# Kernel tuning notes

Hardware: AMD Instinct MI355X
Metric: run time of the kernel (lower is better)

The kernel has to match this reference:

```python
import jax, jax.numpy as jnp
import numpy as np

B, S, IN_DIM, OUT_DIM, HID = 16, 256, 128, 128, 512


def setup_inputs() -> dict:
    key = jax.random.key(0)
    ks = jax.random.split(key, 7)
    x = jax.random.normal(ks[0], (B, S, IN_DIM), dtype=jnp.float32)
    # hypernet linear 1: input_dim -> hyper_hidden_dim
    W1 = jax.random.normal(ks[1], (IN_DIM, HID), dtype=jnp.float32) / np.sqrt(IN_DIM)
    b1 = jax.random.normal(ks[2], (HID,), dtype=jnp.float32) * 0.01
    # hypernet linear 2: hyper_hidden_dim -> input_dim * output_dim
    W2 = jax.random.normal(ks[3], (HID, IN_DIM * OUT_DIM), dtype=jnp.float32) / np.sqrt(HID)
    b2 = jax.random.normal(ks[4], (IN_DIM * OUT_DIM,), dtype=jnp.float32) * 0.01
    # final fc: output_dim -> output_dim
    Wfc = jax.random.normal(ks[5], (OUT_DIM, OUT_DIM), dtype=jnp.float32) / np.sqrt(OUT_DIM)
    bfc = jax.random.normal(ks[6], (OUT_DIM,), dtype=jnp.float32) * 0.01
    return {"x": x, "W1": W1, "b1": b1, "W2": W2, "b2": b2, "Wfc": Wfc, "bfc": bfc}


def reference(x, W1, b1, W2, b2, Wfc, bfc):
    # hypernet: per-token generated weight matrix Wx [B,S,IN,OUT]
    h = jax.nn.relu(jnp.einsum('bsi,ih->bsh', x, W1) + b1)
    Wx = (jnp.einsum('bsh,ho->bso', h, W2) + b2).reshape(x.shape[0], x.shape[1], IN_DIM, OUT_DIM)
    # batched vector-matrix product per (b,s), then sum over s -> [B, OUT]
    y = jnp.einsum('bsi,bsio->bo', x, Wx)
    return y @ Wfc + bfc
```

## Files before the change

### kernel.cpp

```cpp
#include <hip/hip_runtime.h>


typedef __attribute__((ext_vector_type(8))) short     s16x8;
typedef __attribute__((ext_vector_type(8))) unsigned short u16x8;
typedef __attribute__((ext_vector_type(4))) float     f32x4;

__device__ __forceinline__ unsigned short f2bf(float f) {
    union { float f; unsigned int u; } v; v.f = f;
    unsigned int r = v.u + 0x7FFFu + ((v.u >> 16) & 1u);
    return (unsigned short)(r >> 16);
}
__device__ __forceinline__ float bf2f(unsigned short u) {
    union { unsigned int u; float f; } v; v.u = ((unsigned int)u) << 16;
    return v.f;
}

#define OFF_MP   0
#define OFF_PART 2097152
#define OFF_SXP  3145728

__global__ __launch_bounds__(256) void k_AB(const float* __restrict__ x,
        const float* __restrict__ W1, const float* __restrict__ b1,
        float* __restrict__ Mp, float* __restrict__ sxp) {
    __shared__ unsigned short xA[128][136];
    __shared__ unsigned short Ws[128][136];
    __shared__ unsigned short xTl[128][136];
    __shared__ float Wt[128][33];
    __shared__ float b1s[128];
    const int tid = threadIdx.x;
    const int b = blockIdx.x >> 3, sh = (blockIdx.x >> 2) & 1, hb = blockIdx.x & 3;

    {
        const int r = tid >> 1, q = tid & 1;
        const float* xrow = &x[(size_t)(b * 256 + sh * 128 + r) * 128 + q * 64];
        #pragma unroll
        for (int m = 0; m < 8; ++m) {
            const float4 v0 = *(const float4*)&xrow[m * 8];
            const float4 v1 = *(const float4*)&xrow[m * 8 + 4];
            unsigned short t8[8] __attribute__((aligned(16))) = {
                f2bf(v0.x), f2bf(v0.y), f2bf(v0.z), f2bf(v0.w),
                f2bf(v1.x), f2bf(v1.y), f2bf(v1.z), f2bf(v1.w)};
            *(u16x8*)&xA[r][q * 64 + m * 8] = *(u16x8*)t8;
        }
        if (tid < 128) b1s[tid] = b1[hb * 128 + tid];
    }
    for (int hq = 0; hq < 4; ++hq) {
        __syncthreads();
        #pragma unroll
        for (int p = 0; p < 16; ++p) {
            const int flat = p * 256 + tid;
            const int i = flat >> 5, hc = flat & 31;
            Wt[i][hc] = W1[(size_t)i * 512 + hb * 128 + hq * 32 + hc];
        }
        __syncthreads();
        {
            const int h2 = tid >> 3, pt = tid & 7;
            unsigned short t16[16] __attribute__((aligned(16)));
            #pragma unroll
            for (int m = 0; m < 16; ++m)
                t16[m] = f2bf(Wt[pt * 16 + m][h2]);
            *(u16x8*)&Ws[hq * 32 + h2][pt * 16]     = *(u16x8*)&t16[0];
            *(u16x8*)&Ws[hq * 32 + h2][pt * 16 + 8] = *(u16x8*)&t16[8];
        }
    }
    __syncthreads();

    const int w = tid >> 6, lane = tid & 63;
    const int wr = w >> 1, wc = w & 1;
    const int l15 = lane & 15, kl = lane >> 4;
    f32x4 zero = {0.f, 0.f, 0.f, 0.f};

    f32x4 acc[4][4];
    #pragma unroll
    for (int i = 0; i < 4; ++i)
        #pragma unroll
        for (int j = 0; j < 4; ++j) acc[i][j] = zero;
    #pragma unroll
    for (int ks = 0; ks < 4; ++ks) {
        s16x8 a[4], bb[4];
        #pragma unroll
        for (int f = 0; f < 4; ++f) {
            a[f]  = *(const s16x8*)&xA[wr * 64 + f * 16 + l15][ks * 32 + kl * 8];
            bb[f] = *(const s16x8*)&Ws[wc * 64 + f * 16 + l15][ks * 32 + kl * 8];
        }
        #pragma unroll
        for (int fr = 0; fr < 4; ++fr)
            #pragma unroll
            for (int fc = 0; fc < 4; ++fc)
                acc[fr][fc] = __builtin_amdgcn_mfma_f32_16x16x32_bf16(a[fr], bb[fc], acc[fr][fc], 0, 0, 0);
    }
    __syncthreads();

    {
        const int i = tid >> 1, q = tid & 1;
        float sacc = 0.f;
        unsigned short t64[64] __attribute__((aligned(16)));
        #pragma unroll
        for (int m = 0; m < 64; ++m) {
            const unsigned short u = xA[q * 64 + m][i];
            sacc += bf2f(u);
            t64[m] = u;
        }
        #pragma unroll
        for (int v = 0; v < 8; ++v)
            *(u16x8*)&xTl[i][q * 64 + v * 8] = *(u16x8*)&t64[v * 8];
        if (hb == 0)
            sxp[(size_t)((sh * 2 + q) * 16 + b) * 128 + i] = sacc;
    }
    __syncthreads();

    unsigned short (*hts)[136] = xA;
    #pragma unroll
    for (int fr = 0; fr < 4; ++fr)
        #pragma unroll
        for (int fc = 0; fc < 4; ++fc)
            #pragma unroll
            for (int j = 0; j < 4; ++j) {
                const int tok = wr * 64 + fr * 16 + kl * 4 + j;
                const int hid = wc * 64 + fc * 16 + l15;
                const float v = acc[fr][fc][j] + b1s[hid];
                hts[hid][tok] = f2bf(v > 0.f ? v : 0.f);
            }
    __syncthreads();

    f32x4 acc2[4][4];
    #pragma unroll
    for (int i = 0; i < 4; ++i)
        #pragma unroll
        for (int j = 0; j < 4; ++j) acc2[i][j] = zero;
    #pragma unroll
    for (int ks = 0; ks < 4; ++ks) {
        s16x8 a[4], bb[4];
        #pragma unroll
        for (int f = 0; f < 4; ++f) {
            a[f]  = *(const s16x8*)&hts[wr * 64 + f * 16 + l15][ks * 32 + kl * 8];
            bb[f] = *(const s16x8*)&xTl[wc * 64 + f * 16 + l15][ks * 32 + kl * 8];
        }
        #pragma unroll
        for (int fr = 0; fr < 4; ++fr)
            #pragma unroll
            for (int fc = 0; fc < 4; ++fc)
                acc2[fr][fc] = __builtin_amdgcn_mfma_f32_16x16x32_bf16(a[fr], bb[fc], acc2[fr][fc], 0, 0, 0);
    }
    const size_t mpbase = (size_t)sh * (16 * 65536) + (size_t)b * 65536;
    #pragma unroll
    for (int fr = 0; fr < 4; ++fr)
        #pragma unroll
        for (int fc = 0; fc < 4; ++fc)
            #pragma unroll
            for (int j = 0; j < 4; ++j) {
                const int h = hb * 128 + wr * 64 + fr * 16 + kl * 4 + j;
                const int i = wc * 64 + fc * 16 + l15;
                Mp[mpbase + (size_t)h * 128 + i] = acc2[fr][fc][j];
            }
}

__global__ __launch_bounds__(256) void k_C(const float* __restrict__ Mp,
        const float* __restrict__ W2, float* __restrict__ part) {
    __shared__ float Ms[16][128];
    const int tid = threadIdx.x;
    const int p = blockIdx.x;
    const int k0 = p * 128;
    #pragma unroll
    for (int r = 0; r < 8; ++r) {
        const int flat = r * 256 + tid;
        const int b = flat >> 7, kk = flat & 127;
        Ms[b][kk] = Mp[(size_t)b * 65536 + k0 + kk]
                  + Mp[(size_t)(16 + b) * 65536 + k0 + kk];
    }
    __syncthreads();
    const int o2 = (tid & 63) * 2;
    const int g  = tid >> 6;
    float acc[4][2] = {};
    #pragma unroll 8
    for (int kk = 0; kk < 128; ++kk) {
        const float2 w = *(const float2*)&W2[(size_t)(k0 + kk) * 128 + o2];
        #pragma unroll
        for (int bb = 0; bb < 4; ++bb) {
            const float m = Ms[g * 4 + bb][kk];
            acc[bb][0] += m * w.x;
            acc[bb][1] += m * w.y;
        }
    }
    #pragma unroll
    for (int bb = 0; bb < 4; ++bb) {
        float2 v = {acc[bb][0], acc[bb][1]};
        *(float2*)&part[(size_t)(p * 16 + g * 4 + bb) * 128 + o2] = v;
    }
}

__global__ __launch_bounds__(1024) void k_D(const float* __restrict__ part,
        const float* __restrict__ sxp, const float* __restrict__ b2,
        const float* __restrict__ Wfc, const float* __restrict__ bfc,
        float* __restrict__ out) {
    __shared__ float sh[8][128];
    __shared__ float sxs[128];
    __shared__ float ysum[128];
    __shared__ float ysh[128];
    const int b = blockIdx.x;
    const int t = threadIdx.x & 127;
    const int g = threadIdx.x >> 7;
    float y = 0.f;
    #pragma unroll 8
    for (int pp = g * 64; pp < g * 64 + 64; ++pp)
        y += part[(size_t)(pp * 16 + b) * 128 + t];
    sh[g][t] = y;
    __syncthreads();
    if (g == 0) {
        float yy = sh[0][t];
        #pragma unroll
        for (int j = 1; j < 8; ++j) yy += sh[j][t];
        ysum[t] = yy;
        sxs[t] = sxp[(size_t)(0 * 16 + b) * 128 + t] + sxp[(size_t)(1 * 16 + b) * 128 + t]
               + sxp[(size_t)(2 * 16 + b) * 128 + t] + sxp[(size_t)(3 * 16 + b) * 128 + t];
    }
    __syncthreads();
    float yb = 0.f;
    #pragma unroll
    for (int i = g * 16; i < g * 16 + 16; ++i)
        yb += sxs[i] * b2[i * 128 + t];
    sh[g][t] = yb;
    __syncthreads();
    if (g == 0) {
        float yy = ysum[t];
        #pragma unroll
        for (int j = 0; j < 8; ++j) yy += sh[j][t];
        ysh[t] = yy;
    }
    __syncthreads();
    float f = 0.f;
    #pragma unroll
    for (int oo = g * 16; oo < g * 16 + 16; ++oo)
        f += ysh[oo] * Wfc[oo * 128 + t];
    sh[g][t] = f;
    __syncthreads();
    if (g == 0) {
        float s = bfc[t];
        #pragma unroll
        for (int j = 0; j < 8; ++j) s += sh[j][t];
        out[b * 128 + t] = s;
    }
}

extern "C" void kernel_launch(void* const* d_in, const int* in_sizes, int n_in,
                              void* d_out, int out_size, void* d_ws, size_t ws_size,
                              hipStream_t stream) {
    const float* x   = (const float*)d_in[0];
    const float* W1  = (const float*)d_in[1];
    const float* b1  = (const float*)d_in[2];
    const float* W2  = (const float*)d_in[3];
    const float* b2  = (const float*)d_in[4];
    const float* Wfc = (const float*)d_in[5];
    const float* bfc = (const float*)d_in[6];
    float* ws  = (float*)d_ws;
    float* Mp   = ws + OFF_MP;
    float* part = ws + OFF_PART;
    float* sxp  = ws + OFF_SXP;
    float* out  = (float*)d_out;

    k_AB<<<128, 256, 0, stream>>>(x, W1, b1, Mp, sxp);
    k_C <<<512, 256, 0, stream>>>(Mp, W2, part);
    k_D <<<16, 1024, 0, stream>>>(part, sxp, b2, Wfc, bfc, out);
}
```

Before: 34.75 us.

## Split hidden dim finer in k_AB, alias shared memory, vectorize k_C W2 loads

k_AB now gives each block 64 hidden units instead of 128, doubling the grid to 256 blocks so the GPU's many CUs are better filled. Shared buffers are packed into one aliased byte array (Wt overlaps xTl, hts overlaps Ws) to shrink LDS per block. k_C switches to float4 W2 loads with 2 batches per thread instead of float2 with 4. The trade-off is that the x tile load, transpose and bf16 conversion are now repeated in twice as many blocks.

```diff
diff --git a/kernel.cpp b/kernel.cpp
--- a/kernel.cpp
+++ b/kernel.cpp
@@ -22,13 +22,18 @@
 __global__ __launch_bounds__(256) void k_AB(const float* __restrict__ x,
         const float* __restrict__ W1, const float* __restrict__ b1,
         float* __restrict__ Mp, float* __restrict__ sxp) {
-    __shared__ unsigned short xA[128][136];
-    __shared__ unsigned short Ws[128][136];
-    __shared__ unsigned short xTl[128][136];
-    __shared__ float Wt[128][33];
-    __shared__ float b1s[128];
+    __shared__ __align__(16) unsigned char smem[87296];
+    auto Ws  = (unsigned short (*)[136])(smem);
+    auto xA  = (unsigned short (*)[136])(smem + 17408);
+    auto xTl = (unsigned short (*)[136])(smem + 52224);
+    auto Wt  = (float (*)[33])(smem + 52224);
+    float* b1s = (float*)(smem + 87040);
+    auto hts = (unsigned short (*)[136])(smem);
+
     const int tid = threadIdx.x;
-    const int b = blockIdx.x >> 3, sh = (blockIdx.x >> 2) & 1, hb = blockIdx.x & 3;
+    const int b  = blockIdx.x >> 4;
+    const int hb = (blockIdx.x >> 1) & 7;
+    const int sh = blockIdx.x & 1;
 
     {
         const int r = tid >> 1, q = tid & 1;
@@ -42,15 +47,15 @@
                 f2bf(v1.x), f2bf(v1.y), f2bf(v1.z), f2bf(v1.w)};
             *(u16x8*)&xA[r][q * 64 + m * 8] = *(u16x8*)t8;
         }
-        if (tid < 128) b1s[tid] = b1[hb * 128 + tid];
-    }
-    for (int hq = 0; hq < 4; ++hq) {
+        if (tid < 64) b1s[tid] = b1[hb * 64 + tid];
+    }
+    for (int hq = 0; hq < 2; ++hq) {
         __syncthreads();
         #pragma unroll
         for (int p = 0; p < 16; ++p) {
             const int flat = p * 256 + tid;
             const int i = flat >> 5, hc = flat & 31;
-            Wt[i][hc] = W1[(size_t)i * 512 + hb * 128 + hq * 32 + hc];
+            Wt[i][hc] = W1[(size_t)i * 512 + hb * 64 + hq * 32 + hc];
         }
         __syncthreads();
         {
@@ -70,23 +75,24 @@
     const int l15 = lane & 15, kl = lane >> 4;
     f32x4 zero = {0.f, 0.f, 0.f, 0.f};
 
-    f32x4 acc[4][4];
+    f32x4 acc[4][2];
     #pragma unroll
     for (int i = 0; i < 4; ++i)
         #pragma unroll
-        for (int j = 0; j < 4; ++j) acc[i][j] = zero;
+        for (int j = 0; j < 2; ++j) acc[i][j] = zero;
     #pragma unroll
     for (int ks = 0; ks < 4; ++ks) {
-        s16x8 a[4], bb[4];
-        #pragma unroll
-        for (int f = 0; f < 4; ++f) {
-            a[f]  = *(const s16x8*)&xA[wr * 64 + f * 16 + l15][ks * 32 + kl * 8];
-            bb[f] = *(const s16x8*)&Ws[wc * 64 + f * 16 + l15][ks * 32 + kl * 8];
-        }
+        s16x8 a[4], bb[2];
+        #pragma unroll
+        for (int f = 0; f < 4; ++f)
+            a[f] = *(const s16x8*)&xA[wr * 64 + f * 16 + l15][ks * 32 + kl * 8];
+        #pragma unroll
+        for (int f = 0; f < 2; ++f)
+            bb[f] = *(const s16x8*)&Ws[wc * 32 + f * 16 + l15][ks * 32 + kl * 8];
         #pragma unroll
         for (int fr = 0; fr < 4; ++fr)
             #pragma unroll
-            for (int fc = 0; fc < 4; ++fc)
+            for (int fc = 0; fc < 2; ++fc)
                 acc[fr][fc] = __builtin_amdgcn_mfma_f32_16x16x32_bf16(a[fr], bb[fc], acc[fr][fc], 0, 0, 0);
     }
     __syncthreads();
@@ -109,47 +115,47 @@
     }
     __syncthreads();
 
-    unsigned short (*hts)[136] = xA;
     #pragma unroll
     for (int fr = 0; fr < 4; ++fr)
         #pragma unroll
-        for (int fc = 0; fc < 4; ++fc)
+        for (int fc = 0; fc < 2; ++fc)
             #pragma unroll
             for (int j = 0; j < 4; ++j) {
                 const int tok = wr * 64 + fr * 16 + kl * 4 + j;
-                const int hid = wc * 64 + fc * 16 + l15;
+                const int hid = wc * 32 + fc * 16 + l15;
                 const float v = acc[fr][fc][j] + b1s[hid];
                 hts[hid][tok] = f2bf(v > 0.f ? v : 0.f);
             }
     __syncthreads();
 
-    f32x4 acc2[4][4];
-    #pragma unroll
-    for (int i = 0; i < 4; ++i)
+    f32x4 acc2[2][4];
+    #pragma unroll
+    for (int i = 0; i < 2; ++i)
         #pragma unroll
         for (int j = 0; j < 4; ++j) acc2[i][j] = zero;
     #pragma unroll
     for (int ks = 0; ks < 4; ++ks) {
-        s16x8 a[4], bb[4];
-        #pragma unroll
-        for (int f = 0; f < 4; ++f) {
-            a[f]  = *(const s16x8*)&hts[wr * 64 + f * 16 + l15][ks * 32 + kl * 8];
-            bb[f] = *(const s16x8*)&xTl[wc * 64 + f * 16 + l15][ks * 32 + kl * 8];
-        }
-        #pragma unroll
-        for (int fr = 0; fr < 4; ++fr)
+        s16x8 a2[2], b2f[4];
+        #pragma unroll
+        for (int f = 0; f < 2; ++f)
+            a2[f] = *(const s16x8*)&hts[wr * 32 + f * 16 + l15][ks * 32 + kl * 8];
+        #pragma unroll
+        for (int f = 0; f < 4; ++f)
+            b2f[f] = *(const s16x8*)&xTl[wc * 64 + f * 16 + l15][ks * 32 + kl * 8];
+        #pragma unroll
+        for (int fr = 0; fr < 2; ++fr)
             #pragma unroll
             for (int fc = 0; fc < 4; ++fc)
-                acc2[fr][fc] = __builtin_amdgcn_mfma_f32_16x16x32_bf16(a[fr], bb[fc], acc2[fr][fc], 0, 0, 0);
-    }
-    const size_t mpbase = (size_t)sh * (16 * 65536) + (size_t)b * 65536;
-    #pragma unroll
-    for (int fr = 0; fr < 4; ++fr)
+                acc2[fr][fc] = __builtin_amdgcn_mfma_f32_16x16x32_bf16(a2[fr], b2f[fc], acc2[fr][fc], 0, 0, 0);
+    }
+    const size_t mpbase = (size_t)(sh * 16 + b) * 65536;
+    #pragma unroll
+    for (int fr = 0; fr < 2; ++fr)
         #pragma unroll
         for (int fc = 0; fc < 4; ++fc)
             #pragma unroll
             for (int j = 0; j < 4; ++j) {
-                const int h = hb * 128 + wr * 64 + fr * 16 + kl * 4 + j;
+                const int h = hb * 64 + wr * 32 + fr * 16 + kl * 4 + j;
                 const int i = wc * 64 + fc * 16 + l15;
                 Mp[mpbase + (size_t)h * 128 + i] = acc2[fr][fc][j];
             }
@@ -169,24 +175,18 @@
                   + Mp[(size_t)(16 + b) * 65536 + k0 + kk];
     }
     __syncthreads();
-    const int o2 = (tid & 63) * 2;
-    const int g  = tid >> 6;
-    float acc[4][2] = {};
+    const int o4 = (tid & 31) * 4;
+    const int g  = tid >> 5;
+    float4 a0 = {0.f, 0.f, 0.f, 0.f}, a1 = a0;
     #pragma unroll 8
     for (int kk = 0; kk < 128; ++kk) {
-        const float2 w = *(const float2*)&W2[(size_t)(k0 + kk) * 128 + o2];
-        #pragma unroll
-        for (int bb = 0; bb < 4; ++bb) {
-            const float m = Ms[g * 4 + bb][kk];
-            acc[bb][0] += m * w.x;
-            acc[bb][1] += m * w.y;
-        }
-    }
-    #pragma unroll
-    for (int bb = 0; bb < 4; ++bb) {
-        float2 v = {acc[bb][0], acc[bb][1]};
-        *(float2*)&part[(size_t)(p * 16 + g * 4 + bb) * 128 + o2] = v;
-    }
+        const float4 wv = *(const float4*)&W2[(size_t)(k0 + kk) * 128 + o4];
+        const float m0 = Ms[g * 2][kk], m1 = Ms[g * 2 + 1][kk];
+        a0.x += m0 * wv.x; a0.y += m0 * wv.y; a0.z += m0 * wv.z; a0.w += m0 * wv.w;
+        a1.x += m1 * wv.x; a1.y += m1 * wv.y; a1.z += m1 * wv.z; a1.w += m1 * wv.w;
+    }
+    *(float4*)&part[(size_t)(p * 16 + g * 2) * 128 + o4]     = a0;
+    *(float4*)&part[(size_t)(p * 16 + g * 2 + 1) * 128 + o4] = a1;
 }
 
 __global__ __launch_bounds__(1024) void k_D(const float* __restrict__ part,
@@ -258,7 +258,7 @@
     float* sxp  = ws + OFF_SXP;
     float* out  = (float*)d_out;
 
-    k_AB<<<128, 256, 0, stream>>>(x, W1, b1, Mp, sxp);
+    k_AB<<<256, 256, 0, stream>>>(x, W1, b1, Mp, sxp);
     k_C <<<512, 256, 0, stream>>>(Mp, W2, part);
     k_D <<<16, 1024, 0, stream>>>(part, sxp, b2, Wfc, bfc, out);
 }
```

After: 34.70 us. Within noise of the previous version (-0.2%).
